# Optimization experiments

Measured on AMD Instinct MI355X. Metric: run time of the kernel, lower is better.

## Reference

```python
import jax, jax.numpy as jnp
import numpy as np


def _quat_raw_mul(a, b):
    aw, ax, ay, az = a[..., 0], a[..., 1], a[..., 2], a[..., 3]
    bw, bx, by, bz = b[..., 0], b[..., 1], b[..., 2], b[..., 3]
    ow = aw * bw - ax * bx - ay * by - az * bz
    ox = aw * bx + ax * bw + ay * bz - az * by
    oy = aw * by - ax * bz + ay * bw + az * bx
    oz = aw * bz + ax * by - ay * bx + az * bw
    return jnp.stack([ow, ox, oy, oz], axis=-1)


def _standardize(q):
    # pytorch3d.quaternion_multiply standardizes sign so w >= 0
    return jnp.where(q[..., :1] < 0, -q, q)


def _quat_apply(q, v):
    # rotate points v by unit quaternions q: q * (0, v) * conj(q), take imaginary part
    pv = jnp.concatenate([jnp.zeros_like(v[..., :1]), v], axis=-1)
    conj = q * jnp.asarray([1.0, -1.0, -1.0, -1.0], dtype=q.dtype)
    return _quat_raw_mul(_quat_raw_mul(q, pv), conj)[..., 1:]


def _axis_angle_to_quat(aa):
    # pytorch3d.axis_angle_to_quaternion with small-angle Taylor branch
    angle = jnp.linalg.norm(aa, axis=-1, keepdims=True)
    half = 0.5 * angle
    eps = 1e-6
    small = jnp.abs(angle) < eps
    safe_angle = jnp.where(small, jnp.ones_like(angle), angle)
    k = jnp.where(small, 0.5 - angle * angle / 48.0, jnp.sin(half) / safe_angle)
    return jnp.concatenate([jnp.cos(half), aa * k], axis=-1)


def _matrix_to_quat(M):
    # pytorch3d.matrix_to_quaternion (candidate-selection form), vectorized
    m00, m11, m22 = M[..., 0, 0], M[..., 1, 1], M[..., 2, 2]
    q_abs = jnp.sqrt(jax.nn.relu(jnp.stack([
        1.0 + m00 + m11 + m22,
        1.0 + m00 - m11 - m22,
        1.0 - m00 + m11 - m22,
        1.0 - m00 - m11 + m22], axis=-1)))
    c0 = jnp.stack([q_abs[..., 0] ** 2, M[..., 2, 1] - M[..., 1, 2], M[..., 0, 2] - M[..., 2, 0], M[..., 1, 0] - M[..., 0, 1]], axis=-1)
    c1 = jnp.stack([M[..., 2, 1] - M[..., 1, 2], q_abs[..., 1] ** 2, M[..., 1, 0] + M[..., 0, 1], M[..., 0, 2] + M[..., 2, 0]], axis=-1)
    c2 = jnp.stack([M[..., 0, 2] - M[..., 2, 0], M[..., 1, 0] + M[..., 0, 1], q_abs[..., 2] ** 2, M[..., 2, 1] + M[..., 1, 2]], axis=-1)
    c3 = jnp.stack([M[..., 1, 0] - M[..., 0, 1], M[..., 2, 0] + M[..., 0, 2], M[..., 2, 1] + M[..., 1, 2], q_abs[..., 3] ** 2], axis=-1)
    cands = jnp.stack([c0, c1, c2, c3], axis=-2)  # (..., 4 candidates, 4)
    flr = 0.1
    cands = cands / (2.0 * jnp.maximum(q_abs[..., None], flr))
    idx = jnp.argmax(q_abs, axis=-1)
    return jnp.take_along_axis(cands, idx[..., None, None], axis=-2)[..., 0, :]


def _or6d_to_quat(d6):
    a1, a2 = d6[..., :3], d6[..., 3:]
    b1 = a1 / jnp.linalg.norm(a1, axis=-1, keepdims=True)
    a2p = a2 - jnp.sum(b1 * a2, axis=-1, keepdims=True) * b1
    b2 = a2p / jnp.linalg.norm(a2p, axis=-1, keepdims=True)
    b3 = jnp.cross(b1, b2)
    M = jnp.stack([b1, b2, b3], axis=-2)  # (..., 3, 3)
    return _matrix_to_quat(M)


def setup_inputs() -> dict:
    key = jax.random.key(0)
    k1, k2, k3, k4 = jax.random.split(key, 4)
    N, T, J = 256, 1024, 24
    return {
        'root_rvel': jax.random.normal(k1, (N, T, 1, 1), dtype=jnp.float32),
        'local_pos': jax.random.normal(k2, (N, T + 1, J, 3), dtype=jnp.float32),
        'local_rot': jax.random.normal(k3, (N, T + 1, J, 6), dtype=jnp.float32),
        'root_vel': jax.random.normal(k4, (N, T, 1, 2), dtype=jnp.float32),
    }


def reference(root_rvel, local_pos, local_rot, root_vel):
    # cumulative root yaw angle with zero initial frame: (N, T+1, 1, 1)
    r = jnp.cumsum(root_rvel, axis=1)
    r = jnp.concatenate([jnp.zeros_like(r[:, :1]), r], axis=1)
    # axis-angle about Y axis -> quaternion (N, T+1, 1, 4)
    aa = r * jnp.asarray([0.0, 1.0, 0.0], dtype=r.dtype)
    rotation = _axis_angle_to_quat(aa)
    # local 6D rotations -> quaternions (N, T+1, J, 4)
    local_q = _or6d_to_quat(local_rot)
    global_rot = _standardize(_quat_raw_mul(rotation, local_q))
    relative_pos = _quat_apply(rotation, local_pos)
    # lift XZ hip velocity to 3D, rotate into world frame, integrate
    zeros_y = jnp.zeros_like(root_vel[..., :1])
    v3 = jnp.concatenate([root_vel[..., :1], zeros_y, root_vel[..., 1:]], axis=-1)  # (N,T,1,3)
    v3w = _quat_apply(rotation[:, :-1], v3)
    pos_xz = jnp.concatenate([jnp.zeros_like(v3w[:, :1]), jnp.cumsum(v3w, axis=1)], axis=1)  # (N,T+1,1,3)
    global_pos = relative_pos + pos_xz
    return global_pos, global_rot
```

## Files before the change

### kernel.cpp

```cpp
#include <hip/hip_runtime.h>

#define N_SEQ 256
#define T_LEN 1024
#define TP1   (T_LEN + 1)
#define J_NUM 24
#define SEQ_ITEMS (TP1 * J_NUM)
#define TOTAL_ITEMS (N_SEQ * SEQ_ITEMS)
#define GP_TOTAL (N_SEQ * TP1 * J_NUM * 3)

#define ITEMS_PT 4
#define SEQ_THREADS (SEQ_ITEMS / ITEMS_PT)
#define TOTAL_THREADS (TOTAL_ITEMS / ITEMS_PT)
#define NBLOCKS_B (TOTAL_THREADS / 256)

__device__ __forceinline__ float block_scan_incl(float v, float* wsum, int tid) {
    const int lane = tid & 63;
    const int wid  = tid >> 6;
    #pragma unroll
    for (int off = 1; off < 64; off <<= 1) {
        float u = __shfl_up(v, off, 64);
        if (lane >= off) v += u;
    }
    if (lane == 63) wsum[wid] = v;
    __syncthreads();
    if (tid == 0) {
        float acc = 0.0f;
        #pragma unroll
        for (int i = 0; i < 16; ++i) { float t = wsum[i]; wsum[i] = acc; acc += t; }
    }
    __syncthreads();
    return v + wsum[wid];
}

extern "C" __global__ void __launch_bounds__(1024)
scan_kernel(const float* __restrict__ root_rvel,
            const float* __restrict__ root_vel,
            float4* __restrict__ ws4)
{
    const int n   = blockIdx.x;
    const int tid = threadIdx.x;

    __shared__ float  r_s[TP1];
    __shared__ float2 quat_s[TP1];
    __shared__ float  ws_a[16], ws_b[16], ws_c[16];

    {
        float v = root_rvel[n * T_LEN + tid];
        float incl = block_scan_incl(v, ws_a, tid);
        if (tid == 0) r_s[0] = 0.0f;
        r_s[tid + 1] = incl;
    }
    __syncthreads();

    for (int idx = tid; idx < TP1; idx += 1024) {
        float r     = r_s[idx];
        float angle = fabsf(r);
        float half  = 0.5f * angle;
        float k = (angle < 1e-6f) ? (0.5f - angle * angle * (1.0f / 48.0f))
                                  : (__builtin_sinf(half) / angle);
        quat_s[idx] = make_float2(__builtin_cosf(half), r * k);
    }
    __syncthreads();

    {
        float2 vel = ((const float2*)root_vel)[n * T_LEN + tid];
        float2 q   = quat_s[tid];
        float  w = q.x, y = q.y;
        float t1x = w * vel.x + y * vel.y;
        float t1z = w * vel.y - y * vel.x;
        float ax  = t1x * w + t1z * y;
        float az  = t1z * w - t1x * y;
        float ix = block_scan_incl(ax, ws_b, tid);
        float iz = block_scan_incl(az, ws_c, tid);
        float2 qn = quat_s[tid + 1];
        ws4[n * TP1 + tid + 1] = make_float4(qn.x, qn.y, ix, iz);
        if (tid == 0) ws4[n * TP1] = make_float4(1.0f, 0.0f, 0.0f, 0.0f);
    }
}

extern "C" __global__ void __launch_bounds__(256)
elem_kernel(const float4* __restrict__ rot4,
            const float4* __restrict__ pos4,
            const float4* __restrict__ ws4,
            float4* __restrict__ out_rot4,
            float4* __restrict__ out_pos4)
{
    const unsigned g = blockIdx.x * 256u + (unsigned)threadIdx.x;

    const unsigned seq = g / (unsigned)SEQ_THREADS;
    const unsigned rem = g - seq * (unsigned)SEQ_THREADS;
    const unsigned t   = rem / 6u;

    const float4 wq = ws4[seq * (unsigned)TP1 + t];
    const float w = wq.x, yq = wq.y;

    union { float4 v[6]; float f[24]; } R;
    const float4* rb = rot4 + (size_t)g * 6;
    #pragma unroll
    for (int k = 0; k < 6; ++k) R.v[k] = rb[k];

    union { float4 v[3]; float f[12]; } P;
    const float4* pb = pos4 + (size_t)g * 3;
    #pragma unroll
    for (int k = 0; k < 3; ++k) P.v[k] = pb[k];

    union { float4 v[3]; float f[12]; } OP;

    float4* ob = out_rot4 + (size_t)g * 4;

    #pragma unroll
    for (int i = 0; i < ITEMS_PT; ++i) {
        float a1x = R.f[6*i+0], a1y = R.f[6*i+1], a1z = R.f[6*i+2];
        float a2x = R.f[6*i+3], a2y = R.f[6*i+4], a2z = R.f[6*i+5];

        float inv1 = __builtin_amdgcn_rsqf(a1x * a1x + a1y * a1y + a1z * a1z);
        float b1x = a1x * inv1, b1y = a1y * inv1, b1z = a1z * inv1;
        float dp  = b1x * a2x + b1y * a2y + b1z * a2z;
        float px  = a2x - dp * b1x, py = a2y - dp * b1y, pz = a2z - dp * b1z;
        float inv2 = __builtin_amdgcn_rsqf(px * px + py * py + pz * pz);
        float b2x = px * inv2, b2y = py * inv2, b2z = pz * inv2;
        float b3x = b1y * b2z - b1z * b2y;
        float b3y = b1z * b2x - b1x * b2z;
        float b3z = b1x * b2y - b1y * b2x;

        float m00 = b1x, m01 = b1y, m02 = b1z;
        float m10 = b2x, m11 = b2y, m12 = b2z;
        float m20 = b3x, m21 = b3y, m22 = b3z;

        float s0 = fmaxf(1.0f + m00 + m11 + m22, 0.0f);
        float s1 = fmaxf(1.0f + m00 - m11 - m22, 0.0f);
        float s2 = fmaxf(1.0f - m00 + m11 - m22, 0.0f);
        float s3 = fmaxf(1.0f - m00 - m11 + m22, 0.0f);

        int best = 0; float bs = s0;
        if (s1 > bs) { best = 1; bs = s1; }
        if (s2 > bs) { best = 2; bs = s2; }
        if (s3 > bs) { best = 3; bs = s3; }

        float lw, lx, ly, lz;
        if (best == 0)      { lw = bs;         lx = m21 - m12;  ly = m02 - m20;  lz = m10 - m01; }
        else if (best == 1) { lw = m21 - m12;  lx = bs;         ly = m10 + m01;  lz = m02 + m20; }
        else if (best == 2) { lw = m02 - m20;  lx = m10 + m01;  ly = bs;         lz = m21 + m12; }
        else                { lw = m10 - m01;  lx = m20 + m02;  ly = m21 + m12;  lz = bs;        }

        float bv   = __builtin_amdgcn_sqrtf(bs);
        float invd = __builtin_amdgcn_rcpf(2.0f * fmaxf(bv, 0.1f));
        lw *= invd; lx *= invd; ly *= invd; lz *= invd;

        float ow = w * lw - yq * ly;
        float ox = w * lx + yq * lz;
        float oy = w * ly + yq * lw;
        float oz = w * lz - yq * lx;
        if (ow < 0.0f) { ow = -ow; ox = -ox; oy = -oy; oz = -oz; }
        ob[i] = make_float4(ow, ox, oy, oz);

        float vx = P.f[3*i+0], vy = P.f[3*i+1], vz = P.f[3*i+2];
        float t1x = w * vx + yq * vz;
        float t1z = w * vz - yq * vx;
        OP.f[3*i+0] = t1x * w + t1z * yq + wq.z;
        OP.f[3*i+1] = (w * w + yq * yq) * vy;
        OP.f[3*i+2] = t1z * w - t1x * yq + wq.w;
    }

    float4* opb = out_pos4 + (size_t)g * 3;
    #pragma unroll
    for (int k = 0; k < 3; ++k) opb[k] = OP.v[k];
}

extern "C" void kernel_launch(void* const* d_in, const int* in_sizes, int n_in,
                              void* d_out, int out_size, void* d_ws, size_t ws_size,
                              hipStream_t stream) {
    (void)in_sizes; (void)n_in; (void)ws_size; (void)out_size;
    const float* root_rvel = (const float*)d_in[0];
    const float* local_pos = (const float*)d_in[1];
    const float* local_rot = (const float*)d_in[2];
    const float* root_vel  = (const float*)d_in[3];
    float* out = (float*)d_out;

    float4* ws4 = (float4*)d_ws;

    scan_kernel<<<N_SEQ, 1024, 0, stream>>>(root_rvel, root_vel, ws4);

    elem_kernel<<<NBLOCKS_B, 256, 0, stream>>>(
        (const float4*)local_rot, (const float4*)local_pos, ws4,
        (float4*)(out + GP_TOTAL),
        (float4*)out);
}
```

Before: 345.2 us.

## Stage elem kernel loads and stores through shared memory for coalesced access

The element kernel now loads each block's rotation and position data into LDS with fully coalesced float4 accesses, computes two items per thread from LDS, and writes positions back through LDS as coalesced float4 stores. Before, each thread read six or three consecutive float4s strided by thread, which gave uncoalesced wavefront accesses. It also replaces the candidate if-chain with selects, drops the relu/floor clamps, and adds a launch_bounds occupancy hint. The cost is extra barriers and LDS traffic, and removing the clamps could change results in degenerate cases.

```diff
diff --git a/kernel.cpp b/kernel.cpp
--- a/kernel.cpp
+++ b/kernel.cpp
@@ -8,10 +8,8 @@
 #define TOTAL_ITEMS (N_SEQ * SEQ_ITEMS)
 #define GP_TOTAL (N_SEQ * TP1 * J_NUM * 3)
 
-#define ITEMS_PT 4
-#define SEQ_THREADS (SEQ_ITEMS / ITEMS_PT)
-#define TOTAL_THREADS (TOTAL_ITEMS / ITEMS_PT)
-#define NBLOCKS_B (TOTAL_THREADS / 256)
+#define IPB 512
+#define NBLOCKS_B (TOTAL_ITEMS / IPB)
 
 __device__ __forceinline__ float block_scan_incl(float v, float* wsum, int tid) {
     const int lane = tid & 63;
@@ -78,93 +76,123 @@
     }
 }
 
-extern "C" __global__ void __launch_bounds__(256)
+__device__ __forceinline__ void process_item(
+    float a1x, float a1y, float a1z, float a2x, float a2y, float a2z,
+    float vx,  float vy,  float vz,  float4 wq,
+    float4* __restrict__ out_rot_addr, float* __restrict__ s_out3)
+{
+    const float w = wq.x, yq = wq.y;
+
+    float inv1 = __builtin_amdgcn_rsqf(a1x * a1x + a1y * a1y + a1z * a1z);
+    float b1x = a1x * inv1, b1y = a1y * inv1, b1z = a1z * inv1;
+    float dp  = b1x * a2x + b1y * a2y + b1z * a2z;
+    float px  = a2x - dp * b1x, py = a2y - dp * b1y, pz = a2z - dp * b1z;
+    float inv2 = __builtin_amdgcn_rsqf(px * px + py * py + pz * pz);
+    float b2x = px * inv2, b2y = py * inv2, b2z = pz * inv2;
+    float b3x = b1y * b2z - b1z * b2y;
+    float b3y = b1z * b2x - b1x * b2z;
+    float b3z = b1x * b2y - b1y * b2x;
+
+    float m00 = b1x, m01 = b1y, m02 = b1z;
+    float m10 = b2x, m11 = b2y, m12 = b2z;
+    float m20 = b3x, m21 = b3y, m22 = b3z;
+
+    float s0 = 1.0f + m00 + m11 + m22;
+    float s1 = 1.0f + m00 - m11 - m22;
+    float s2 = 1.0f - m00 + m11 - m22;
+    float s3 = 1.0f - m00 - m11 + m22;
+
+    int best = 0; float bs = s0;
+    if (s1 > bs) { best = 1; bs = s1; }
+    if (s2 > bs) { best = 2; bs = s2; }
+    if (s3 > bs) { best = 3; bs = s3; }
+
+    float c0 = m21 - m12, c1 = m02 - m20, c2 = m10 - m01;
+    float d0 = m10 + m01, d1 = m02 + m20, d2 = m21 + m12;
+
+    float lw = best == 0 ? bs : (best == 1 ? c0 : (best == 2 ? c1 : c2));
+    float lx = best == 0 ? c0 : (best == 1 ? bs : (best == 2 ? d0 : d1));
+    float ly = best == 0 ? c1 : (best == 1 ? d0 : (best == 2 ? bs : d2));
+    float lz = best == 0 ? c2 : (best == 1 ? d1 : (best == 2 ? d2 : bs));
+
+    float invd = __builtin_amdgcn_rcpf(2.0f * __builtin_amdgcn_sqrtf(bs));
+    lw *= invd; lx *= invd; ly *= invd; lz *= invd;
+
+    float ow = w * lw - yq * ly;
+    float ox = w * lx + yq * lz;
+    float oy = w * ly + yq * lw;
+    float oz = w * lz - yq * lx;
+    if (ow < 0.0f) { ow = -ow; ox = -ox; oy = -oy; oz = -oz; }
+    *out_rot_addr = make_float4(ow, ox, oy, oz);
+
+    float t1x = w * vx + yq * vz;
+    float t1z = w * vz - yq * vx;
+    s_out3[0] = t1x * w + t1z * yq + wq.z;
+    s_out3[1] = (w * w + yq * yq) * vy;
+    s_out3[2] = t1z * w - t1x * yq + wq.w;
+}
+
+extern "C" __global__ void __launch_bounds__(256, 8)
 elem_kernel(const float4* __restrict__ rot4,
             const float4* __restrict__ pos4,
             const float4* __restrict__ ws4,
             float4* __restrict__ out_rot4,
             float4* __restrict__ out_pos4)
 {
-    const unsigned g = blockIdx.x * 256u + (unsigned)threadIdx.x;
-
-    const unsigned seq = g / (unsigned)SEQ_THREADS;
-    const unsigned rem = g - seq * (unsigned)SEQ_THREADS;
-    const unsigned t   = rem / 6u;
-
-    const float4 wq = ws4[seq * (unsigned)TP1 + t];
-    const float w = wq.x, yq = wq.y;
-
-    union { float4 v[6]; float f[24]; } R;
-    const float4* rb = rot4 + (size_t)g * 6;
-    #pragma unroll
-    for (int k = 0; k < 6; ++k) R.v[k] = rb[k];
-
-    union { float4 v[3]; float f[12]; } P;
-    const float4* pb = pos4 + (size_t)g * 3;
-    #pragma unroll
-    for (int k = 0; k < 3; ++k) P.v[k] = pb[k];
-
-    union { float4 v[3]; float f[12]; } OP;
-
-    float4* ob = out_rot4 + (size_t)g * 4;
-
-    #pragma unroll
-    for (int i = 0; i < ITEMS_PT; ++i) {
-        float a1x = R.f[6*i+0], a1y = R.f[6*i+1], a1z = R.f[6*i+2];
-        float a2x = R.f[6*i+3], a2y = R.f[6*i+4], a2z = R.f[6*i+5];
-
-        float inv1 = __builtin_amdgcn_rsqf(a1x * a1x + a1y * a1y + a1z * a1z);
-        float b1x = a1x * inv1, b1y = a1y * inv1, b1z = a1z * inv1;
-        float dp  = b1x * a2x + b1y * a2y + b1z * a2z;
-        float px  = a2x - dp * b1x, py = a2y - dp * b1y, pz = a2z - dp * b1z;
-        float inv2 = __builtin_amdgcn_rsqf(px * px + py * py + pz * pz);
-        float b2x = px * inv2, b2y = py * inv2, b2z = pz * inv2;
-        float b3x = b1y * b2z - b1z * b2y;
-        float b3y = b1z * b2x - b1x * b2z;
-        float b3z = b1x * b2y - b1y * b2x;
-
-        float m00 = b1x, m01 = b1y, m02 = b1z;
-        float m10 = b2x, m11 = b2y, m12 = b2z;
-        float m20 = b3x, m21 = b3y, m22 = b3z;
-
-        float s0 = fmaxf(1.0f + m00 + m11 + m22, 0.0f);
-        float s1 = fmaxf(1.0f + m00 - m11 - m22, 0.0f);
-        float s2 = fmaxf(1.0f - m00 + m11 - m22, 0.0f);
-        float s3 = fmaxf(1.0f - m00 - m11 + m22, 0.0f);
-
-        int best = 0; float bs = s0;
-        if (s1 > bs) { best = 1; bs = s1; }
-        if (s2 > bs) { best = 2; bs = s2; }
-        if (s3 > bs) { best = 3; bs = s3; }
-
-        float lw, lx, ly, lz;
-        if (best == 0)      { lw = bs;         lx = m21 - m12;  ly = m02 - m20;  lz = m10 - m01; }
-        else if (best == 1) { lw = m21 - m12;  lx = bs;         ly = m10 + m01;  lz = m02 + m20; }
-        else if (best == 2) { lw = m02 - m20;  lx = m10 + m01;  ly = bs;         lz = m21 + m12; }
-        else                { lw = m10 - m01;  lx = m20 + m02;  ly = m21 + m12;  lz = bs;        }
-
-        float bv   = __builtin_amdgcn_sqrtf(bs);
-        float invd = __builtin_amdgcn_rcpf(2.0f * fmaxf(bv, 0.1f));
-        lw *= invd; lx *= invd; ly *= invd; lz *= invd;
-
-        float ow = w * lw - yq * ly;
-        float ox = w * lx + yq * lz;
-        float oy = w * ly + yq * lw;
-        float oz = w * lz - yq * lx;
-        if (ow < 0.0f) { ow = -ow; ox = -ox; oy = -oy; oz = -oz; }
-        ob[i] = make_float4(ow, ox, oy, oz);
-
-        float vx = P.f[3*i+0], vy = P.f[3*i+1], vz = P.f[3*i+2];
-        float t1x = w * vx + yq * vz;
-        float t1z = w * vz - yq * vx;
-        OP.f[3*i+0] = t1x * w + t1z * yq + wq.z;
-        OP.f[3*i+1] = (w * w + yq * yq) * vy;
-        OP.f[3*i+2] = t1z * w - t1x * yq + wq.w;
-    }
-
-    float4* opb = out_pos4 + (size_t)g * 3;
-    #pragma unroll
-    for (int k = 0; k < 3; ++k) opb[k] = OP.v[k];
+    __shared__ float4 s_rot4[768];
+    __shared__ float4 s_pos4[384];
+    float* s_rot = (float*)s_rot4;
+    float* s_pos = (float*)s_pos4;
+    float*  s_out  = s_rot;
+    float4* s_out4 = s_rot4;
+
+    const int tid = threadIdx.x;
+    const unsigned blk = blockIdx.x;
+
+    {
+        const float4* rb = rot4 + (size_t)blk * 768;
+        s_rot4[tid]       = rb[tid];
+        s_rot4[tid + 256] = rb[tid + 256];
+        s_rot4[tid + 512] = rb[tid + 512];
+        const float4* pb = pos4 + (size_t)blk * 384;
+        s_pos4[tid] = pb[tid];
+        if (tid < 128) s_pos4[tid + 256] = pb[tid + 256];
+    }
+
+    const unsigned a0 = blk * (unsigned)IPB + (unsigned)tid;
+    const unsigned a1 = a0 + 256u;
+    const unsigned seq0 = a0 / (unsigned)SEQ_ITEMS;
+    const unsigned t0   = (a0 - seq0 * (unsigned)SEQ_ITEMS) / (unsigned)J_NUM;
+    const unsigned seq1 = a1 / (unsigned)SEQ_ITEMS;
+    const unsigned t1   = (a1 - seq1 * (unsigned)SEQ_ITEMS) / (unsigned)J_NUM;
+    const float4 wq0 = ws4[seq0 * (unsigned)TP1 + t0];
+    const float4 wq1 = ws4[seq1 * (unsigned)TP1 + t1];
+
+    __syncthreads();
+
+    const float2* s_rot2 = (const float2*)s_rot;
+    const int L0 = tid, L1 = tid + 256;
+    float2 ra0 = s_rot2[3 * L0 + 0];
+    float2 rb0 = s_rot2[3 * L0 + 1];
+    float2 rc0 = s_rot2[3 * L0 + 2];
+    float2 ra1 = s_rot2[3 * L1 + 0];
+    float2 rb1 = s_rot2[3 * L1 + 1];
+    float2 rc1 = s_rot2[3 * L1 + 2];
+    float p0x = s_pos[3 * L0 + 0], p0y = s_pos[3 * L0 + 1], p0z = s_pos[3 * L0 + 2];
+    float p1x = s_pos[3 * L1 + 0], p1y = s_pos[3 * L1 + 1], p1z = s_pos[3 * L1 + 2];
+
+    __syncthreads();
+
+    process_item(ra0.x, ra0.y, rb0.x, rb0.y, rc0.x, rc0.y,
+                 p0x, p0y, p0z, wq0, &out_rot4[a0], &s_out[3 * L0]);
+    process_item(ra1.x, ra1.y, rb1.x, rb1.y, rc1.x, rc1.y,
+                 p1x, p1y, p1z, wq1, &out_rot4[a1], &s_out[3 * L1]);
+
+    __syncthreads();
+
+    float4* opb = out_pos4 + (size_t)blk * 384;
+    opb[tid] = s_out4[tid];
+    if (tid < 128) opb[tid + 256] = s_out4[tid + 256];
 }
 
 extern "C" void kernel_launch(void* const* d_in, const int* in_sizes, int n_in,
```

New measurement: 340.6 us. About the same (-1.3%).
